# Performance work log

Measured on AMD Instinct MI355X. Metric: run time of the kernel, lower is better.

Reference implementation:

```python
import jax, jax.numpy as jnp
import numpy as np

SCALE = 64.0
MARGIN = 0.5
EPS_CLAMP = 1e-7
EPS_NORM = 1e-12

N, D, C = 4096, 512, 30000


def setup_inputs() -> dict:
    key = jax.random.key(0)
    k1, k2, k3 = jax.random.split(key, 3)
    embeddings = jax.random.normal(k1, (N, D), dtype=jnp.float32)
    classifier_weights = jax.random.normal(k2, (C, D), dtype=jnp.float32)
    labels = jax.random.randint(k3, (N,), 0, C, dtype=jnp.int64)
    return {"embeddings": embeddings, "labels": labels, "classifier_weights": classifier_weights}


def reference(embeddings, labels, classifier_weights):
    # F.normalize(classifier_weights): L2-normalize each class row (dim=1)
    norm = jnp.linalg.norm(classifier_weights, axis=1, keepdims=True)
    w_norm = classifier_weights / jnp.maximum(norm, EPS_NORM)
    # cosine similarity logits: [N, C]  (embeddings are NOT normalized in source)
    cosine = jnp.einsum("nd,cd->nc", embeddings, w_norm)
    # angle with margin added only at the target class
    angle = jnp.arccos(jnp.clip(cosine, -1.0 + EPS_CLAMP, 1.0 - EPS_CLAMP))
    one_hot = jax.nn.one_hot(labels, C, dtype=cosine.dtype)
    logits = jnp.cos(angle + MARGIN * one_hot) * SCALE
    # mean cross-entropy
    logp = jax.nn.log_softmax(logits, axis=-1)
    nll = -jnp.take_along_axis(logp, labels[:, None], axis=1)[:, 0]
    return jnp.mean(nll)
```

## Files before the change

### kernel.cpp

```cpp
#include <hip/hip_runtime.h>
#include <cstdint>
#include <cstddef>

#define N_ROWS 4096
#define DIM    512
#define NCLS   30000
#define BM 256
#define BN 256
#define BK 32
#define NT2  118
#define CPAD (NT2 * 256)
#define SPT 2
#define NSTRIPS (NT2 / SPT)
#define KT  (DIM / BK)
#define NS  (SPT * KT)

typedef float  f32x4  __attribute__((ext_vector_type(4)));
typedef short  bf16x8 __attribute__((ext_vector_type(8)));
typedef unsigned int   u32;
typedef unsigned short u16;

#define WB_BYTES   ((size_t)CPAD * DIM * 2)
#define EB_BYTES   ((size_t)N_ROWS * DIM * 2)
#define PS_BYTES   ((size_t)NT2 * N_ROWS * 4)
#define CT_BYTES   ((size_t)N_ROWS * 4)
#define BL_BYTES   (64 * 4)
#define LAB_BYTES  ((size_t)N_ROWS * 4)

#define CLIP_HI ( 1.0f - 1e-7f)
#define CLIP_LO (-1.0f + 1e-7f)
#define COSM 0.8775825618903728f
#define SINM 0.4794255386042030f
#define K1   92.33248261972189f

__device__ __forceinline__ u16 f2bf(float f) {
  u32 x = __builtin_bit_cast(u32, f);
  x += 0x7fffu + ((x >> 16) & 1u);
  return (u16)(x >> 16);
}

__device__ __forceinline__ void gl_lds16(const u16* g, u16* l) {
  __builtin_amdgcn_global_load_lds((const __attribute__((address_space(1))) u32*)g,
                                   (__attribute__((address_space(3))) u32*)l,
                                   16, 0, 0);
}

__global__ void lab_detect(const int* __restrict__ lab, int* __restrict__ flag) {
  __shared__ int s_nz;
  int tid = threadIdx.x;
  if (tid == 0) s_nz = 0;
  __syncthreads();
  int nz = 0;
  for (int i = tid; i < N_ROWS / 2; i += 1024) nz |= lab[2 * i + 1];
  if (nz) atomicOr(&s_nz, 1);
  __syncthreads();
  if (tid == 0) *flag = (s_nz == 0) ? 1 : 0;
}

__global__ void lab_fix(const int* __restrict__ lab, const int* __restrict__ flag,
                        int* __restrict__ out) {
  int i = blockIdx.x * 256 + threadIdx.x;
  out[i] = flag[0] ? lab[2 * i] : lab[i];
}

__global__ void prep_w(const float* __restrict__ w, u16* __restrict__ wb) {
  int wv   = threadIdx.x >> 6;
  int lane = threadIdx.x & 63;
  int c = blockIdx.x * 4 + wv;
  u16* dst = wb + (size_t)c * DIM + lane * 8;
  if (c >= NCLS) {
    *(uint4*)dst = make_uint4(0, 0, 0, 0);
    return;
  }
  const float* src = w + (size_t)c * DIM + lane * 8;
  float4 v0 = *(const float4*)src;
  float4 v1 = *(const float4*)(src + 4);
  float a[8] = {v0.x, v0.y, v0.z, v0.w, v1.x, v1.y, v1.z, v1.w};
  float ss = 0.f;
  #pragma unroll
  for (int i = 0; i < 8; i++) ss += a[i] * a[i];
  #pragma unroll
  for (int off = 32; off; off >>= 1) ss += __shfl_xor(ss, off, 64);
  float inv = 1.0f / fmaxf(sqrtf(ss), 1e-12f);
  union { u16 h[8]; uint4 q; } pk;
  #pragma unroll
  for (int i = 0; i < 8; i++) pk.h[i] = f2bf(a[i] * inv);
  *(uint4*)dst = pk.q;
}

__global__ void prep_e(const float* __restrict__ e, u16* __restrict__ eb) {
  size_t idx = ((size_t)blockIdx.x * 256 + threadIdx.x) * 8;
  float4 v0 = *(const float4*)(e + idx);
  float4 v1 = *(const float4*)(e + idx + 4);
  float a[8] = {v0.x, v0.y, v0.z, v0.w, v1.x, v1.y, v1.z, v1.w};
  union { u16 h[8]; uint4 q; } pk;
  #pragma unroll
  for (int i = 0; i < 8; i++) pk.h[i] = f2bf(a[i]);
  *(uint4*)(eb + idx) = pk.q;
}

__global__ void tgt_k(const float* __restrict__ emb, const float* __restrict__ wts,
                      const int* __restrict__ lab, float* __restrict__ ct) {
  int w = threadIdx.x >> 6, l = threadIdx.x & 63;
  int row = blockIdx.x * 4 + w;
  int c = lab[row];
  const float* e  = emb + (size_t)row * DIM + l * 8;
  const float* wp = wts + (size_t)c   * DIM + l * 8;
  float4 e0 = *(const float4*)e,       e1 = *(const float4*)(e + 4);
  float4 w0 = *(const float4*)wp,      w1 = *(const float4*)(wp + 4);
  float dot = e0.x*w0.x + e0.y*w0.y + e0.z*w0.z + e0.w*w0.w
            + e1.x*w1.x + e1.y*w1.y + e1.z*w1.z + e1.w*w1.w;
  float ss  = w0.x*w0.x + w0.y*w0.y + w0.z*w0.z + w0.w*w0.w
            + w1.x*w1.x + w1.y*w1.y + w1.z*w1.z + w1.w*w1.w;
  #pragma unroll
  for (int off = 32; off; off >>= 1) {
    dot += __shfl_xor(dot, off, 64);
    ss  += __shfl_xor(ss,  off, 64);
  }
  if (l == 0) ct[row] = dot / fmaxf(sqrtf(ss), 1e-12f);
}

__global__ __launch_bounds__(512, 1) void arc_main(
    const u16* __restrict__ eb, const u16* __restrict__ wb,
    float* __restrict__ psum)
{
  __shared__ __align__(16) u16 lds[6 * 8192];
  __shared__ float ep[4][BM];
  const int tid = threadIdx.x;
  const int l   = tid & 63;
  const int w   = tid >> 6;
  const int wm  = w >> 2, wn = w & 3;

  const int bid = blockIdx.x;
  const int wg  = (bid & 7) * (16 * NSTRIPS / 8) + (bid >> 3);
  const int mi    = wg & 15;
  const int strip = wg >> 4;
  const int rowbase = mi * BM;
  const int n0s = strip * SPT;

  u32 aoff[8], boff[4];
  const int bq = l >> 4;
  #pragma unroll
  for (int m = 0; m < 8; m++) {
    int r = wm * 128 + m * 16 + (l & 15);
    aoff[m] = (u32)r * BK + ((bq ^ ((r >> 1) & 3)) << 3);
  }
  #pragma unroll
  for (int n = 0; n < 4; n++) {
    int r = wn * 64 + n * 16 + (l & 15);
    boff[n] = (u32)r * BK + ((bq ^ ((r >> 1) & 3)) << 3);
  }

  u32 goff[2];
  #pragma unroll
  for (int c = 0; c < 2; c++) {
    int rl = c * 128 + (tid >> 2);
    goff[c] = (u32)rl * DIM + (((tid & 3) ^ ((rl >> 1) & 3)) << 3);
  }
  const u16* ebR = eb + (size_t)rowbase * DIM;

  u16 *pA = lds,             *qA = lds + 8192,  *sA = lds + 16384;
  u16 *pB = lds + 24576,     *qB = lds + 32768, *sB = lds + 40960;

  #define STAGE_A(v_, t_, c_) \
    gl_lds16(ebR + (u32)(((v_) & 15) * BK) + goff[c_], (t_) + (c_) * 4096 + w * 512)
  #define STAGE_B(v_, t_, c_) \
    gl_lds16(wb + (u32)(n0s + ((v_) >> 4)) * (BN * DIM) + (u32)(((v_) & 15) * BK) + goff[c_], \
             (t_) + (c_) * 4096 + w * 512)

  f32x4 acc[8][4];
  #pragma unroll
  for (int m = 0; m < 8; m++)
    #pragma unroll
    for (int n = 0; n < 4; n++)
      #pragma unroll
      for (int q = 0; q < 4; q++) acc[m][n][q] = 0.f;

  STAGE_A(0, pA, 0); STAGE_A(0, pA, 1); STAGE_B(0, pB, 0); STAGE_B(0, pB, 1);
  STAGE_A(1, qA, 0); STAGE_A(1, qA, 1); STAGE_B(1, qB, 0); STAGE_B(1, qB, 1);

  for (int u = 0; u < NS; u++) {
    const bool st = (u + 2 < NS);
    if (u < NS - 1) asm volatile("s_waitcnt vmcnt(4)" ::: "memory");
    else            asm volatile("s_waitcnt vmcnt(0)" ::: "memory");
    __builtin_amdgcn_s_barrier();
    asm volatile("" ::: "memory");

    bf16x8 af[8], bg[4];
    #pragma unroll
    for (int m = 0; m < 4; m++) af[m] = *(const bf16x8*)&pA[aoff[m]];
    #pragma unroll
    for (int n = 0; n < 4; n++) bg[n] = *(const bf16x8*)&pB[boff[n]];
    if (st) { STAGE_A(u + 2, sA, 0); STAGE_A(u + 2, sA, 1); }
    __builtin_amdgcn_s_setprio(1);
    #pragma unroll
    for (int m = 0; m < 4; m++)
      #pragma unroll
      for (int n = 0; n < 4; n++)
        acc[m][n] = __builtin_amdgcn_mfma_f32_16x16x32_bf16(af[m], bg[n], acc[m][n], 0, 0, 0);
    __builtin_amdgcn_s_setprio(0);
    __builtin_amdgcn_s_barrier();
    asm volatile("" ::: "memory");

    #pragma unroll
    for (int m = 0; m < 4; m++) af[m + 4] = *(const bf16x8*)&pA[aoff[m + 4]];
    if (st) { STAGE_B(u + 2, sB, 0); STAGE_B(u + 2, sB, 1); }
    __builtin_amdgcn_s_setprio(1);
    #pragma unroll
    for (int m = 0; m < 4; m++)
      #pragma unroll
      for (int n = 0; n < 4; n++)
        acc[m + 4][n] = __builtin_amdgcn_mfma_f32_16x16x32_bf16(af[m + 4], bg[n], acc[m + 4][n], 0, 0, 0);
    __builtin_amdgcn_s_setprio(0);

    if ((u & 15) == 15) {
      const int nt = n0s + (u >> 4);
      #pragma unroll
      for (int m = 0; m < 8; m++) {
        #pragma unroll
        for (int q = 0; q < 4; q++) {
          float s = 0.f;
          #pragma unroll
          for (int n = 0; n < 4; n++) {
            float tc = __builtin_amdgcn_fmed3f(acc[m][n][q], CLIP_LO, CLIP_HI);
            s += __builtin_amdgcn_exp2f(__builtin_fmaf(tc, K1, -K1));
            acc[m][n][q] = 0.f;
          }
          s += __shfl_xor(s, 1, 64);
          s += __shfl_xor(s, 2, 64);
          s += __shfl_xor(s, 4, 64);
          s += __shfl_xor(s, 8, 64);
          if ((l & 15) == 0) ep[wn][wm * 128 + m * 16 + (l >> 4) * 4 + q] = s;
        }
      }
      asm volatile("s_waitcnt lgkmcnt(0)" ::: "memory");
      __builtin_amdgcn_s_barrier();
      asm volatile("" ::: "memory");
      if (l < 32) {
        int r = w * 32 + l;
        float t = ep[0][r] + ep[1][r] + ep[2][r] + ep[3][r];
        psum[(size_t)nt * N_ROWS + rowbase + r] = t;
      }
      __builtin_amdgcn_s_barrier();
    }

    u16* t0 = pA; pA = qA; qA = sA; sA = t0;
    u16* t1 = pB; pB = qB; qB = sB; sB = t1;
  }
  #undef STAGE_A
  #undef STAGE_B
}

__global__ void arc_finish1(const float* __restrict__ psum, const float* __restrict__ ct,
                            float* __restrict__ bl) {
  int tid = threadIdx.x;
  int row = blockIdx.x * 256 + tid;
  float S = 0.f;
  for (int p = 0; p < NT2; p++) S += psum[(size_t)p * N_ROWS + row];
  float c  = __builtin_amdgcn_fmed3f(ct[row], CLIP_LO, CLIP_HI);
  float cm = c * COSM - sqrtf(fmaxf(1.0f - c * c, 0.0f)) * SINM;
  float S2 = S - __builtin_amdgcn_exp2f(__builtin_fmaf(c,  K1, -K1))
               + __builtin_amdgcn_exp2f(__builtin_fmaf(cm, K1, -K1));
  float loss = 64.0f + __builtin_amdgcn_logf(S2) * 0.6931471805599453f - 64.0f * cm;
  #pragma unroll
  for (int off = 32; off; off >>= 1) loss += __shfl_xor(loss, off, 64);
  __shared__ float red[4];
  if ((tid & 63) == 0) red[tid >> 6] = loss;
  __syncthreads();
  if (tid == 0) bl[blockIdx.x] = red[0] + red[1] + red[2] + red[3];
}

__global__ void arc_finish2(const float* __restrict__ bl, float* __restrict__ out) {
  if (threadIdx.x == 0) {
    float t = 0.f;
    for (int i = 0; i < N_ROWS / 256; i++) t += bl[i];
    out[0] = t * (1.0f / (float)N_ROWS);
  }
}

extern "C" void kernel_launch(void* const* d_in, const int* in_sizes, int n_in,
                              void* d_out, int out_size, void* d_ws, size_t ws_size,
                              hipStream_t stream) {
  const float* emb   = (const float*)d_in[0];
  const int*   lab   = (const int*)d_in[1];
  const float* wts   = (const float*)d_in[2];

  char* ws = (char*)d_ws;
  u16*   wb    = (u16*)(ws);
  u16*   eb    = (u16*)(ws + WB_BYTES);
  float* psum  = (float*)(ws + WB_BYTES + EB_BYTES);
  float* ct    = (float*)(ws + WB_BYTES + EB_BYTES + PS_BYTES);
  float* bl    = (float*)(ws + WB_BYTES + EB_BYTES + PS_BYTES + CT_BYTES);
  int*   lab32 = (int*)  (ws + WB_BYTES + EB_BYTES + PS_BYTES + CT_BYTES + BL_BYTES);
  int*   flag  = (int*)  (ws + WB_BYTES + EB_BYTES + PS_BYTES + CT_BYTES + BL_BYTES + LAB_BYTES);

  lab_detect<<<dim3(1), dim3(1024), 0, stream>>>(lab, flag);
  lab_fix<<<dim3(N_ROWS / 256), dim3(256), 0, stream>>>(lab, flag, lab32);
  prep_w<<<dim3(CPAD / 4), dim3(256), 0, stream>>>(wts, wb);
  prep_e<<<dim3((N_ROWS * DIM / 8) / 256), dim3(256), 0, stream>>>(emb, eb);
  tgt_k<<<dim3(N_ROWS / 4), dim3(256), 0, stream>>>(emb, wts, lab32, ct);
  arc_main<<<dim3(16 * NSTRIPS), dim3(512), 0, stream>>>(eb, wb, psum);
  arc_finish1<<<dim3(N_ROWS / 256), dim3(256), 0, stream>>>(psum, ct, bl);
  arc_finish2<<<dim3(1), dim3(64), 0, stream>>>(bl, (float*)d_out);
}
```

Baseline: 211.1 us.

## Load A fragments directly from global into registers, double-buffer B with BK=64

```diff
diff --git a/kernel.cpp b/kernel.cpp
--- a/kernel.cpp
+++ b/kernel.cpp
@@ -7,7 +7,7 @@
 #define NCLS   30000
 #define BM 256
 #define BN 256
-#define BK 32
+#define BK 64
 #define NT2  118
 #define CPAD (NT2 * 256)
 #define SPT 2
@@ -124,49 +124,39 @@
     const u16* __restrict__ eb, const u16* __restrict__ wb,
     float* __restrict__ psum)
 {
-  __shared__ __align__(16) u16 lds[6 * 8192];
+  __shared__ __align__(16) u16 lB[2][BN * BK];
   __shared__ float ep[4][BM];
-  const int tid = threadIdx.x;
-  const int l   = tid & 63;
-  const int w   = tid >> 6;
-  const int wm  = w >> 2, wn = w & 3;
-
-  const int bid = blockIdx.x;
-  const int wg  = (bid & 7) * (16 * NSTRIPS / 8) + (bid >> 3);
-  const int mi    = wg & 15;
-  const int strip = wg >> 4;
+  const int t  = threadIdx.x;
+  const int l  = t & 63;
+  const int w  = t >> 6;
+  const int wm = w >> 2, wn = w & 3;
+  const int cl = l & 15, bq = l >> 4;
+  const int mi    = blockIdx.x & 15;
+  const int strip = blockIdx.x >> 4;
   const int rowbase = mi * BM;
   const int n0s = strip * SPT;
 
-  u32 aoff[8], boff[4];
-  const int bq = l >> 4;
-  #pragma unroll
-  for (int m = 0; m < 8; m++) {
-    int r = wm * 128 + m * 16 + (l & 15);
-    aoff[m] = (u32)r * BK + ((bq ^ ((r >> 1) & 3)) << 3);
-  }
-  #pragma unroll
-  for (int n = 0; n < 4; n++) {
-    int r = wn * 64 + n * 16 + (l & 15);
-    boff[n] = (u32)r * BK + ((bq ^ ((r >> 1) & 3)) << 3);
-  }
-
-  u32 goff[2];
-  #pragma unroll
-  for (int c = 0; c < 2; c++) {
-    int rl = c * 128 + (tid >> 2);
-    goff[c] = (u32)rl * DIM + (((tid & 3) ^ ((rl >> 1) & 3)) << 3);
-  }
+  u32 au[8];
+  #pragma unroll
+  for (int m = 0; m < 8; m++)
+    au[m] = (u32)(wm * 128 + m * 16 + cl) * DIM + bq * 8;
   const u16* ebR = eb + (size_t)rowbase * DIM;
 
-  u16 *pA = lds,             *qA = lds + 8192,  *sA = lds + 16384;
-  u16 *pB = lds + 24576,     *qB = lds + 32768, *sB = lds + 40960;
-
-  #define STAGE_A(v_, t_, c_) \
-    gl_lds16(ebR + (u32)(((v_) & 15) * BK) + goff[c_], (t_) + (c_) * 4096 + w * 512)
-  #define STAGE_B(v_, t_, c_) \
-    gl_lds16(wb + (u32)(n0s + ((v_) >> 4)) * (BN * DIM) + (u32)(((v_) & 15) * BK) + goff[c_], \
-             (t_) + (c_) * 4096 + w * 512)
+  u32 boff[8];
+  #pragma unroll
+  for (int s = 0; s < 2; s++)
+    #pragma unroll
+    for (int n = 0; n < 4; n++) {
+      int r = wn * 64 + n * 16 + cl;
+      boff[s * 4 + n] = (u32)r * BK + (((s * 4 + bq) ^ (r & 7)) << 3);
+    }
+
+  u32 goff[4];
+  #pragma unroll
+  for (int c = 0; c < 4; c++) {
+    int rl = c * 64 + (t >> 3);
+    goff[c] = (u32)rl * DIM + (((t & 7) ^ (rl & 7)) << 3);
+  }
 
   f32x4 acc[8][4];
   #pragma unroll
@@ -176,45 +166,72 @@
       #pragma unroll
       for (int q = 0; q < 4; q++) acc[m][n][q] = 0.f;
 
-  STAGE_A(0, pA, 0); STAGE_A(0, pA, 1); STAGE_B(0, pB, 0); STAGE_B(0, pB, 1);
-  STAGE_A(1, qA, 0); STAGE_A(1, qA, 1); STAGE_B(1, qB, 0); STAGE_B(1, qB, 1);
+  {
+    const u32 bb0 = (u32)n0s * (BN * DIM);
+    #pragma unroll
+    for (int c = 0; c < 4; c++)
+      gl_lds16(wb + bb0 + goff[c], &lB[0][c * 4096 + w * 512]);
+  }
 
   for (int u = 0; u < NS; u++) {
-    const bool st = (u + 2 < NS);
-    if (u < NS - 1) asm volatile("s_waitcnt vmcnt(4)" ::: "memory");
-    else            asm volatile("s_waitcnt vmcnt(0)" ::: "memory");
+    const u16* Bs = &lB[u & 1][0];
+    u16* Bn = &lB[(u + 1) & 1][0];
+    const bool st = (u + 1 < NS);
+    const u32 ka  = (u32)(u & 7) * BK;
+    const u32 bbn = (u32)(n0s + ((u + 1) >> 3)) * (BN * DIM) + (u32)((u + 1) & 7) * BK;
+
+    asm volatile("s_waitcnt vmcnt(0)" ::: "memory");
     __builtin_amdgcn_s_barrier();
     asm volatile("" ::: "memory");
 
-    bf16x8 af[8], bg[4];
-    #pragma unroll
-    for (int m = 0; m < 4; m++) af[m] = *(const bf16x8*)&pA[aoff[m]];
-    #pragma unroll
-    for (int n = 0; n < 4; n++) bg[n] = *(const bf16x8*)&pB[boff[n]];
-    if (st) { STAGE_A(u + 2, sA, 0); STAGE_A(u + 2, sA, 1); }
+    uint4  av[8];
+    bf16x8 bg[4];
+
+    #pragma unroll
+    for (int m = 0; m < 8; m++)
+      av[m] = *(const uint4*)(ebR + au[m] + ka);
+    asm volatile("" ::: "memory");
+    if (st) {
+      gl_lds16(wb + bbn + goff[0], &Bn[0 * 4096 + w * 512]);
+      gl_lds16(wb + bbn + goff[1], &Bn[1 * 4096 + w * 512]);
+    }
+    asm volatile("" ::: "memory");
+    #pragma unroll
+    for (int n = 0; n < 4; n++) bg[n] = *(const bf16x8*)&Bs[boff[n]];
+    asm volatile("s_waitcnt vmcnt(2)" ::: "memory");
     __builtin_amdgcn_s_setprio(1);
     #pragma unroll
-    for (int m = 0; m < 4; m++)
+    for (int m = 0; m < 8; m++)
       #pragma unroll
       for (int n = 0; n < 4; n++)
-        acc[m][n] = __builtin_amdgcn_mfma_f32_16x16x32_bf16(af[m], bg[n], acc[m][n], 0, 0, 0);
+        acc[m][n] = __builtin_amdgcn_mfma_f32_16x16x32_bf16(
+            __builtin_bit_cast(bf16x8, av[m]), bg[n], acc[m][n], 0, 0, 0);
+    __builtin_amdgcn_s_setprio(0);
+
+    #pragma unroll
+    for (int m = 0; m < 8; m++)
+      av[m] = *(const uint4*)(ebR + au[m] + ka + 32);
+    asm volatile("" ::: "memory");
+    if (st) {
+      gl_lds16(wb + bbn + goff[2], &Bn[2 * 4096 + w * 512]);
+      gl_lds16(wb + bbn + goff[3], &Bn[3 * 4096 + w * 512]);
+    }
+    asm volatile("" ::: "memory");
+    #pragma unroll
+    for (int n = 0; n < 4; n++) bg[n] = *(const bf16x8*)&Bs[boff[4 + n]];
+    asm volatile("s_waitcnt vmcnt(2)" ::: "memory");
+    __builtin_amdgcn_s_setprio(1);
+    #pragma unroll
+    for (int m = 0; m < 8; m++)
+      #pragma unroll
+      for (int n = 0; n < 4; n++)
+        acc[m][n] = __builtin_amdgcn_mfma_f32_16x16x32_bf16(
+            __builtin_bit_cast(bf16x8, av[m]), bg[n], acc[m][n], 0, 0, 0);
     __builtin_amdgcn_s_setprio(0);
     __builtin_amdgcn_s_barrier();
-    asm volatile("" ::: "memory");
-
-    #pragma unroll
-    for (int m = 0; m < 4; m++) af[m + 4] = *(const bf16x8*)&pA[aoff[m + 4]];
-    if (st) { STAGE_B(u + 2, sB, 0); STAGE_B(u + 2, sB, 1); }
-    __builtin_amdgcn_s_setprio(1);
-    #pragma unroll
-    for (int m = 0; m < 4; m++)
-      #pragma unroll
-      for (int n = 0; n < 4; n++)
-        acc[m + 4][n] = __builtin_amdgcn_mfma_f32_16x16x32_bf16(af[m + 4], bg[n], acc[m + 4][n], 0, 0, 0);
-    __builtin_amdgcn_s_setprio(0);
-
-    if ((u & 15) == 15) {
-      const int nt = n0s + (u >> 4);
+
+    if ((u & 7) == 7) {
+      const int nt = n0s + (u >> 3);
       #pragma unroll
       for (int m = 0; m < 8; m++) {
         #pragma unroll
@@ -238,17 +255,12 @@
       asm volatile("" ::: "memory");
       if (l < 32) {
         int r = w * 32 + l;
-        float t = ep[0][r] + ep[1][r] + ep[2][r] + ep[3][r];
-        psum[(size_t)nt * N_ROWS + rowbase + r] = t;
+        float v = ep[0][r] + ep[1][r] + ep[2][r] + ep[3][r];
+        psum[(size_t)nt * N_ROWS + rowbase + r] = v;
       }
       __builtin_amdgcn_s_barrier();
     }
-
-    u16* t0 = pA; pA = qA; qA = sA; sA = t0;
-    u16* t1 = pB; pB = qB; qB = sB; sB = t1;
-  }
-  #undef STAGE_A
-  #undef STAGE_B
+  }
 }
 
 __global__ void arc_finish1(const float* __restrict__ psum, const float* __restrict__ ct,
```

Result: slower. 375.0 us (+77.7%).
